# Optimization experiments

Hardware: AMD Instinct MI355X
Metric: run time of the kernel (lower is better)

The kernel has to match this reference:

```python
import jax, jax.numpy as jnp
import numpy as np

B, S, E, H, DK, DV, DF = 4, 2048, 512, 8, 64, 64, 2048
EPS = 1e-3  # keras LayerNormalization default epsilon


def setup_inputs() -> dict:
    key = jax.random.key(0)
    ks = jax.random.split(key, 24)
    def n(k, shape, scale=0.02):
        return jax.random.normal(k, shape, jnp.float32) * scale
    inp = {}
    inp["x"] = jax.random.normal(ks[0], (B, S, E), jnp.float32)
    inp["encoder_output"] = jax.random.normal(ks[1], (B, S, E), jnp.float32)
    # lookahead mask: 1 above the diagonal (masked), broadcast over batch/heads
    inp["lookahead_mask"] = jnp.triu(jnp.ones((S, S), jnp.int32), k=1)[None, None]
    # padding mask: 0 = keep (no padding in this synthetic batch)
    inp["padding_mask"] = jnp.zeros((B, 1, 1, S), jnp.int32)
    # self-attention params
    inp["sa_Wq"] = n(ks[2], (E, H * DK)); inp["sa_bq"] = jnp.zeros((H * DK,), jnp.float32)
    inp["sa_Wk"] = n(ks[3], (E, H * DK)); inp["sa_bk"] = jnp.zeros((H * DK,), jnp.float32)
    inp["sa_Wv"] = n(ks[4], (E, H * DV)); inp["sa_bv"] = jnp.zeros((H * DV,), jnp.float32)
    inp["sa_Wo"] = n(ks[5], (H * DV, E)); inp["sa_bo"] = jnp.zeros((E,), jnp.float32)
    # cross-attention params
    inp["ca_Wq"] = n(ks[6], (E, H * DK)); inp["ca_bq"] = jnp.zeros((H * DK,), jnp.float32)
    inp["ca_Wk"] = n(ks[7], (E, H * DK)); inp["ca_bk"] = jnp.zeros((H * DK,), jnp.float32)
    inp["ca_Wv"] = n(ks[8], (E, H * DV)); inp["ca_bv"] = jnp.zeros((H * DV,), jnp.float32)
    inp["ca_Wo"] = n(ks[9], (H * DV, E)); inp["ca_bo"] = jnp.zeros((E,), jnp.float32)
    # feed-forward params
    inp["ff_W1"] = n(ks[10], (E, DF)); inp["ff_b1"] = jnp.zeros((DF,), jnp.float32)
    inp["ff_W2"] = n(ks[11], (DF, E)); inp["ff_b2"] = jnp.zeros((E,), jnp.float32)
    # layernorm params (3 add&norm blocks)
    for i in (1, 2, 3):
        inp[f"ln{i}_g"] = jnp.ones((E,), jnp.float32)
        inp[f"ln{i}_b"] = jnp.zeros((E,), jnp.float32)
    return inp


def _mha(q_in, k_in, v_in, mask, Wq, bq, Wk, bk, Wv, bv, Wo, bo):
    Bq, Sq, _ = q_in.shape
    Sk = k_in.shape[1]
    q = (q_in @ Wq + bq).reshape(Bq, Sq, H, DK).transpose(0, 2, 1, 3)  # bhqd
    k = (k_in @ Wk + bk).reshape(Bq, Sk, H, DK).transpose(0, 2, 1, 3)  # bhkd
    v = (v_in @ Wv + bv).reshape(Bq, Sk, H, DV).transpose(0, 2, 1, 3)  # bhkd
    scores = jnp.einsum("bhqd,bhkd->bhqk", q, k) / jnp.sqrt(jnp.float32(DK))
    scores = scores - 1e9 * mask.astype(scores.dtype)  # additive mask (1 = masked)
    attn = jax.nn.softmax(scores, axis=-1)
    out = jnp.einsum("bhqk,bhkd->bhqd", attn, v)
    out = out.transpose(0, 2, 1, 3).reshape(Bq, Sq, H * DV)
    return out @ Wo + bo


def _add_norm(x, sub, g, b):
    y = x + sub
    m = jnp.mean(y, axis=-1, keepdims=True)
    v = jnp.var(y, axis=-1, keepdims=True)
    return (y - m) / jnp.sqrt(v + EPS) * g + b


def reference(x, encoder_output, lookahead_mask, padding_mask,
              sa_Wq, sa_bq, sa_Wk, sa_bk, sa_Wv, sa_bv, sa_Wo, sa_bo,
              ca_Wq, ca_bq, ca_Wk, ca_bk, ca_Wv, ca_bv, ca_Wo, ca_bo,
              ff_W1, ff_b1, ff_W2, ff_b2,
              ln1_g, ln1_b, ln2_g, ln2_b, ln3_g, ln3_b):
    # dropout is identity at inference (training=False)
    a1 = _mha(x, x, x, lookahead_mask,
              sa_Wq, sa_bq, sa_Wk, sa_bk, sa_Wv, sa_bv, sa_Wo, sa_bo)
    x1 = _add_norm(x, a1, ln1_g, ln1_b)
    a2 = _mha(x1, encoder_output, encoder_output, padding_mask,
              ca_Wq, ca_bq, ca_Wk, ca_bk, ca_Wv, ca_bv, ca_Wo, ca_bo)
    x2 = _add_norm(x1, a2, ln2_g, ln2_b)
    ff = jax.nn.relu(x2 @ ff_W1 + ff_b1) @ ff_W2 + ff_b2
    return _add_norm(x2, ff, ln3_g, ln3_b)
```

## Files before the change

kernel.cpp:

```cpp
#include <hip/hip_runtime.h>

#define Bx  4
#define Sx  2048
#define Ex  512
#define Hx  8
#define Tt  (Bx * Sx)

typedef short          short8 __attribute__((ext_vector_type(8)));
typedef float          f32x4  __attribute__((ext_vector_type(4)));
typedef unsigned short u16;

__device__ __forceinline__ u16 f2bf(float f) {
    unsigned int u = __float_as_uint(f);
    u += 0x7fffu + ((u >> 16) & 1u);
    return (u16)(u >> 16);
}
__device__ __forceinline__ float bf2f(u16 h) {
    return __uint_as_float(((unsigned int)h) << 16);
}

__global__ __launch_bounds__(256) void f32_to_bf16_2(const float* __restrict__ a,
                                                     const float* __restrict__ b,
                                                     u16* __restrict__ oa,
                                                     u16* __restrict__ ob)
{
    const float* in  = blockIdx.y ? b : a;
    u16*         out = blockIdx.y ? ob : oa;
    int i = (blockIdx.x * 256 + threadIdx.x) << 2;
    float4 v = *(const float4*)(in + i);
    ushort4 o;
    o.x = f2bf(v.x); o.y = f2bf(v.y); o.z = f2bf(v.z); o.w = f2bf(v.w);
    *(ushort4*)(out + i) = o;
}

__global__ __launch_bounds__(256) void transpose_bf16(const float* __restrict__ W,
                                                      u16* __restrict__ Wt,
                                                      int K, int N)
{
    __shared__ u16 tile[32][33];
    const int n0 = blockIdx.x * 32, k0 = blockIdx.y * 32;
    const int tx = threadIdx.x & 31, ty = threadIdx.x >> 5;
#pragma unroll
    for (int i = 0; i < 32; i += 8)
        tile[ty + i][tx] = f2bf(W[(size_t)(k0 + ty + i) * N + n0 + tx]);
    __syncthreads();
#pragma unroll
    for (int i = 0; i < 32; i += 8)
        Wt[(size_t)(n0 + ty + i) * K + k0 + tx] = tile[tx][ty + i];
}

struct WPtrs { const float* w[8]; };
__global__ __launch_bounds__(256) void transpose8_bf16(WPtrs ws, u16* __restrict__ base)
{
    __shared__ u16 tile[32][33];
    const float* W  = ws.w[blockIdx.z];
    u16*         Wt = base + (size_t)blockIdx.z * 262144;
    const int n0 = blockIdx.x * 32, k0 = blockIdx.y * 32;
    const int tx = threadIdx.x & 31, ty = threadIdx.x >> 5;
#pragma unroll
    for (int i = 0; i < 32; i += 8)
        tile[ty + i][tx] = f2bf(W[(size_t)(k0 + ty + i) * 512 + n0 + tx]);
    __syncthreads();
#pragma unroll
    for (int i = 0; i < 32; i += 8)
        Wt[(size_t)(n0 + ty + i) * 512 + k0 + tx] = tile[tx][ty + i];
}

template<int OUT_BF16, int RELU>
__global__ __launch_bounds__(256) void gemm128(const u16* __restrict__ A,
                                               const u16* __restrict__ Bt,
                                               const float* __restrict__ b0,
                                               const float* __restrict__ b1,
                                               const float* __restrict__ b2,
                                               const float* __restrict__ b3,
                                               void* __restrict__ Cout,
                                               int M, int N, int K, int ldc)
{
    __shared__ u16 As[128 * 40];
    __shared__ u16 Bs[128 * 40];

    const int tid  = threadIdx.x;
    const int w    = tid >> 6;
    const int lane = tid & 63;
    const int c    = lane & 15;
    const int quad = lane >> 4;
    const int wr   = w >> 1, wc = w & 1;
    const int m0   = blockIdx.y * 128;
    const int n0   = blockIdx.x * 128;

    const int row0 = tid >> 2;
    const int kc   = (tid & 3) << 3;

    const u16* Ap = A  + (size_t)(m0 + row0) * K + kc;
    const u16* Bp = Bt + (size_t)(n0 + row0) * K + kc;
    const size_t rstep = (size_t)64 * K;

    f32x4 acc[4][4];
#pragma unroll
    for (int i = 0; i < 4; i++)
#pragma unroll
        for (int j = 0; j < 4; j++) { acc[i][j][0]=0.f; acc[i][j][1]=0.f; acc[i][j][2]=0.f; acc[i][j][3]=0.f; }

    short8 ra0 = *(const short8*)(Ap);
    short8 ra1 = *(const short8*)(Ap + rstep);
    short8 rb0 = *(const short8*)(Bp);
    short8 rb1 = *(const short8*)(Bp + rstep);

    for (int k0 = 0; k0 < K; k0 += 32) {
        __syncthreads();
        *(short8*)&As[row0 * 40 + kc]        = ra0;
        *(short8*)&As[(row0 + 64) * 40 + kc] = ra1;
        *(short8*)&Bs[row0 * 40 + kc]        = rb0;
        *(short8*)&Bs[(row0 + 64) * 40 + kc] = rb1;
        __syncthreads();

        if (k0 + 32 < K) {
            ra0 = *(const short8*)(Ap + k0 + 32);
            ra1 = *(const short8*)(Ap + rstep + k0 + 32);
            rb0 = *(const short8*)(Bp + k0 + 32);
            rb1 = *(const short8*)(Bp + rstep + k0 + 32);
        }

        short8 af[4], bf[4];
#pragma unroll
        for (int i = 0; i < 4; i++)
            af[i] = *(const short8*)&As[(wr * 64 + i * 16 + c) * 40 + quad * 8];
#pragma unroll
        for (int j = 0; j < 4; j++)
            bf[j] = *(const short8*)&Bs[(wc * 64 + j * 16 + c) * 40 + quad * 8];
#pragma unroll
        for (int i = 0; i < 4; i++)
#pragma unroll
            for (int j = 0; j < 4; j++)
                acc[i][j] = __builtin_amdgcn_mfma_f32_16x16x32_bf16(af[i], bf[j], acc[i][j], 0, 0, 0);
    }

    const int seg = n0 >> 9;
    const float* bp = seg == 0 ? b0 : (seg == 1 ? b1 : (seg == 2 ? b2 : b3));
    const int nbase = n0 & 511;
    float bv[4];
#pragma unroll
    for (int j = 0; j < 4; j++) bv[j] = bp[nbase + wc * 64 + j * 16 + c];

#pragma unroll
    for (int i = 0; i < 4; i++) {
#pragma unroll
        for (int j = 0; j < 4; j++) {
            int colg = n0 + wc * 64 + j * 16 + c;
#pragma unroll
            for (int r = 0; r < 4; r++) {
                int rowg = m0 + wr * 64 + i * 16 + quad * 4 + r;
                float v = acc[i][j][r] + bv[j];
                if (RELU) v = fmaxf(v, 0.f);
                if (OUT_BF16) ((u16*)Cout)[(size_t)rowg * ldc + colg] = f2bf(v);
                else          ((float*)Cout)[(size_t)rowg * ldc + colg] = v;
            }
        }
    }
}

template<int OUT_BF16, int RELU>
__global__ __launch_bounds__(128) void gemm64(const u16* __restrict__ A,
                                              const u16* __restrict__ Bt,
                                              const float* __restrict__ bias,
                                              void* __restrict__ Cout,
                                              int M, int N, int K, int ldc)
{
    __shared__ u16 As[128 * 40];
    __shared__ u16 Bs[64 * 40];

    const int tid  = threadIdx.x;
    const int w    = tid >> 6;
    const int lane = tid & 63;
    const int c    = lane & 15;
    const int quad = lane >> 4;
    const int m0   = blockIdx.y * 128;
    const int n0   = blockIdx.x * 64;

    const int rA = tid >> 2;
    const int kc = (tid & 3) << 3;

    const u16* Ap = A  + (size_t)(m0 + rA) * K + kc;
    const u16* Bp = Bt + (size_t)(n0 + rA) * K + kc;
    const size_t a32 = (size_t)32 * K;

    f32x4 acc[4][4];
#pragma unroll
    for (int i = 0; i < 4; i++)
#pragma unroll
        for (int j = 0; j < 4; j++) { acc[i][j][0]=0.f; acc[i][j][1]=0.f; acc[i][j][2]=0.f; acc[i][j][3]=0.f; }

    short8 ra[4], rb[2];
#pragma unroll
    for (int i = 0; i < 4; i++) ra[i] = *(const short8*)(Ap + i * a32);
#pragma unroll
    for (int i = 0; i < 2; i++) rb[i] = *(const short8*)(Bp + i * a32);

    for (int k0 = 0; k0 < K; k0 += 32) {
        __syncthreads();
#pragma unroll
        for (int i = 0; i < 4; i++) *(short8*)&As[(rA + i * 32) * 40 + kc] = ra[i];
#pragma unroll
        for (int i = 0; i < 2; i++) *(short8*)&Bs[(rA + i * 32) * 40 + kc] = rb[i];
        __syncthreads();

        if (k0 + 32 < K) {
#pragma unroll
            for (int i = 0; i < 4; i++) ra[i] = *(const short8*)(Ap + i * a32 + k0 + 32);
#pragma unroll
            for (int i = 0; i < 2; i++) rb[i] = *(const short8*)(Bp + i * a32 + k0 + 32);
        }

        short8 af[4], bf[4];
#pragma unroll
        for (int i = 0; i < 4; i++)
            af[i] = *(const short8*)&As[(w * 64 + i * 16 + c) * 40 + quad * 8];
#pragma unroll
        for (int j = 0; j < 4; j++)
            bf[j] = *(const short8*)&Bs[(j * 16 + c) * 40 + quad * 8];
#pragma unroll
        for (int i = 0; i < 4; i++)
#pragma unroll
            for (int j = 0; j < 4; j++)
                acc[i][j] = __builtin_amdgcn_mfma_f32_16x16x32_bf16(af[i], bf[j], acc[i][j], 0, 0, 0);
    }

    float bv[4];
#pragma unroll
    for (int j = 0; j < 4; j++) bv[j] = bias[n0 + j * 16 + c];

#pragma unroll
    for (int i = 0; i < 4; i++) {
#pragma unroll
        for (int j = 0; j < 4; j++) {
            int colg = n0 + j * 16 + c;
#pragma unroll
            for (int r = 0; r < 4; r++) {
                int rowg = m0 + w * 64 + i * 16 + quad * 4 + r;
                float v = acc[i][j][r] + bv[j];
                if (RELU) v = fmaxf(v, 0.f);
                if (OUT_BF16) ((u16*)Cout)[(size_t)rowg * ldc + colg] = f2bf(v);
                else          ((float*)Cout)[(size_t)rowg * ldc + colg] = v;
            }
        }
    }
}

template<bool CAUSAL>
__global__ __launch_bounds__(256) void attn_mfma(const u16* __restrict__ Q,
                                                 const u16* __restrict__ K,
                                                 const u16* __restrict__ V,
                                                 u16* __restrict__ O,
                                                 int ldq, int ldk, int ldv)
{
    __shared__ u16 Klds[2][64 * 72];
    __shared__ u16 Vtlds[2][64 * 72];

    const int tid  = threadIdx.x;
    const int w    = tid >> 6;
    const int lane = tid & 63;
    const int c    = lane & 15;
    const int quad = lane >> 4;

    const int flat = blockIdx.y * 16 + blockIdx.x;
    const int idx  = flat >> 3;
    const int bh   = (flat & 7) * 4 + (idx >> 4);
    const int q0   = (idx & 15) * 128;

    const int b    = bh >> 3;
    const int h    = bh & 7;
    const int bS   = b * Sx;
    const int hoff = h * 64;
    const int qw   = q0 + w * 32;

    const int kkey = tid >> 3;
    const int kc8  = (tid & 7) << 3;
    const int vdim = tid & 63;
    const int vq   = tid >> 6;
    const int vp   = vq << 3;
    int vkey[8];
#pragma unroll
    for (int j = 0; j < 8; j++) vkey[j] = ((j & 4) << 2) + (vq << 2) + (j & 3);

    short8 qa[2][2];
#pragma unroll
    for (int a = 0; a < 2; a++) {
        const u16* qp = Q + (size_t)(bS + qw + a * 16 + c) * ldq + hoff;
        qa[a][0] = *(const short8*)(qp + quad * 8);
        qa[a][1] = *(const short8*)(qp + 32 + quad * 8);
    }

    f32x4 of[2][4];
#pragma unroll
    for (int a = 0; a < 2; a++)
#pragma unroll
        for (int f = 0; f < 4; f++) { of[a][f][0]=0.f; of[a][f][1]=0.f; of[a][f][2]=0.f; of[a][f][3]=0.f; }
    float lpart[2] = {0.f, 0.f};

    const int kend = CAUSAL ? (q0 + 128) : Sx;

    const u16* Kgp = K + (size_t)(bS + kkey) * ldk + hoff + kc8;
    const u16* Vgp = V + (size_t)bS * ldv + hoff + vdim;
    const size_t k32 = (size_t)32 * ldk;

    {
        short8 kr0 = *(const short8*)(Kgp);
        short8 kr1 = *(const short8*)(Kgp + k32);
        union { short8 v; u16 u[8]; } vb0, vb1;
#pragma unroll
        for (int j = 0; j < 8; j++) vb0.u[j] = Vgp[(size_t)vkey[j] * ldv];
#pragma unroll
        for (int j = 0; j < 8; j++) vb1.u[j] = Vgp[(size_t)(32 + vkey[j]) * ldv];
        *(short8*)&Klds[0][kkey * 72 + kc8]        = kr0;
        *(short8*)&Klds[0][(kkey + 32) * 72 + kc8] = kr1;
        *(short8*)&Vtlds[0][vdim * 72 + vp]        = vb0.v;
        *(short8*)&Vtlds[0][vdim * 72 + 32 + vp]   = vb1.v;
    }
    __syncthreads();

    int cur = 0;
    for (int kt = 0; kt < kend; kt += 64) {
        const bool more = (kt + 64 < kend);

        short8 kr0, kr1;
        union { short8 v; u16 u[8]; } vb0, vb1;
        if (more) {
            const u16* kp = Kgp + (size_t)(kt + 64) * ldk;
            kr0 = *(const short8*)(kp);
            kr1 = *(const short8*)(kp + k32);
#pragma unroll
            for (int j = 0; j < 8; j++)
                vb0.u[j] = Vgp[(size_t)(kt + 64 + vkey[j]) * ldv];
#pragma unroll
            for (int j = 0; j < 8; j++)
                vb1.u[j] = Vgp[(size_t)(kt + 96 + vkey[j]) * ldv];
        }

        int fm0 = 4, fm1 = 4;
        if (CAUSAL) {
            int d0 = ((qw + 15 - kt) >> 4) + 1;
            int d1 = ((qw + 31 - kt) >> 4) + 1;
            fm0 = d0 < 0 ? 0 : (d0 > 4 ? 4 : d0);
            fm1 = d1 < 0 ? 0 : (d1 > 4 ? 4 : d1);
        }

        if (fm1 > 0) {
            f32x4 s[2][4];
#pragma unroll
            for (int f = 0; f < 4; f++) {
                if (f < fm1) {
                    short8 kb0 = *(const short8*)&Klds[cur][(f * 16 + c) * 72 + quad * 8];
                    short8 kb1 = *(const short8*)&Klds[cur][(f * 16 + c) * 72 + 32 + quad * 8];
#pragma unroll
                    for (int a = 0; a < 2; a++) {
                        const int fma_ = a ? fm1 : fm0;
                        if (f < fma_) {
                            f32x4 z; z[0]=0.f; z[1]=0.f; z[2]=0.f; z[3]=0.f;
                            z = __builtin_amdgcn_mfma_f32_16x16x32_bf16(kb0, qa[a][0], z, 0, 0, 0);
                            z = __builtin_amdgcn_mfma_f32_16x16x32_bf16(kb1, qa[a][1], z, 0, 0, 0);
                            s[a][f] = z;
                        }
                    }
                }
            }

            union { unsigned int u[4]; short8 s8; } paA[2], paB[2];
#pragma unroll
            for (int a = 0; a < 2; a++) {
                const int fma_ = a ? fm1 : fm0;
                const int qg = qw + a * 16 + c;
#pragma unroll
                for (int f = 0; f < 4; f++) {
                    u16 pb[4];
#pragma unroll
                    for (int r = 0; r < 4; r++) {
                        float p = 0.f;
                        int kg = kt + f * 16 + quad * 4 + r;
                        if (f < fma_ && !(CAUSAL && kg > qg))
                            p = __expf(s[a][f][r] * 0.125f);
                        pb[r] = f2bf(p);
                        lpart[a] += bf2f(pb[r]);
                    }
                    unsigned int w0 = (unsigned int)pb[0] | ((unsigned int)pb[1] << 16);
                    unsigned int w1 = (unsigned int)pb[2] | ((unsigned int)pb[3] << 16);
                    if (f < 2) { paA[a].u[f * 2] = w0; paA[a].u[f * 2 + 1] = w1; }
                    else       { paB[a].u[(f - 2) * 2] = w0; paB[a].u[(f - 2) * 2 + 1] = w1; }
                }
            }

#pragma unroll
            for (int f2 = 0; f2 < 4; f2++) {
                short8 vb0f = *(const short8*)&Vtlds[cur][(f2 * 16 + c) * 72 + quad * 8];
                short8 vb1f = *(const short8*)&Vtlds[cur][(f2 * 16 + c) * 72 + 32 + quad * 8];
                if (fm0 > 0)
                    of[0][f2] = __builtin_amdgcn_mfma_f32_16x16x32_bf16(paA[0].s8, vb0f, of[0][f2], 0, 0, 0);
                of[1][f2] = __builtin_amdgcn_mfma_f32_16x16x32_bf16(paA[1].s8, vb0f, of[1][f2], 0, 0, 0);
                if (fm0 > 2)
                    of[0][f2] = __builtin_amdgcn_mfma_f32_16x16x32_bf16(paB[0].s8, vb1f, of[0][f2], 0, 0, 0);
                if (fm1 > 2)
                    of[1][f2] = __builtin_amdgcn_mfma_f32_16x16x32_bf16(paB[1].s8, vb1f, of[1][f2], 0, 0, 0);
            }
        }

        if (more) {
            *(short8*)&Klds[cur ^ 1][kkey * 72 + kc8]        = kr0;
            *(short8*)&Klds[cur ^ 1][(kkey + 32) * 72 + kc8] = kr1;
            *(short8*)&Vtlds[cur ^ 1][vdim * 72 + vp]        = vb0.v;
            *(short8*)&Vtlds[cur ^ 1][vdim * 72 + 32 + vp]   = vb1.v;
        }
        __syncthreads();
        cur ^= 1;
    }

    float rinv[2][4];
#pragma unroll
    for (int a = 0; a < 2; a++) {
        float D = lpart[a];
        D += __shfl_xor(D, 16, 64);
        D += __shfl_xor(D, 32, 64);
        float rcp = 1.f / D;
#pragma unroll
        for (int r = 0; r < 4; r++)
            rinv[a][r] = __shfl(rcp, quad * 4 + r, 64);
    }

    u16* Ob = O + (size_t)(bS + qw) * Ex + hoff;
#pragma unroll
    for (int a = 0; a < 2; a++)
#pragma unroll
        for (int f = 0; f < 4; f++)
#pragma unroll
            for (int r = 0; r < 4; r++)
                Ob[(size_t)(a * 16 + quad * 4 + r) * Ex + f * 16 + c] =
                    f2bf(of[a][f][r] * rinv[a][r]);
}

__global__ __launch_bounds__(256) void ln_add(const float* __restrict__ x,
                                              const float* __restrict__ s,
                                              const float* __restrict__ g,
                                              const float* __restrict__ bta,
                                              float* __restrict__ out,
                                              u16* __restrict__ out_bf)
{
    __shared__ float red[8];
    const int    row  = blockIdx.x;
    const int    t    = threadIdx.x;
    const size_t base = (size_t)row * Ex;

    float2 xv = *(const float2*)(x + base + (t << 1));
    float2 sv = *(const float2*)(s + base + (t << 1));
    float  y0 = xv.x + sv.x;
    float  y1 = xv.y + sv.y;

    float sum = y0 + y1;
    float sq  = y0 * y0 + y1 * y1;
#pragma unroll
    for (int o = 32; o > 0; o >>= 1) {
        sum += __shfl_down(sum, o, 64);
        sq  += __shfl_down(sq,  o, 64);
    }
    const int wid = t >> 6, lane = t & 63;
    if (lane == 0) { red[wid] = sum; red[4 + wid] = sq; }
    __syncthreads();
    if (t == 0) {
        red[0] = red[0] + red[1] + red[2] + red[3];
        red[4] = red[4] + red[5] + red[6] + red[7];
    }
    __syncthreads();

    const float mean = red[0] * (1.f / 512.f);
    const float var  = red[4] * (1.f / 512.f) - mean * mean;
    const float rstd = rsqrtf(var + 1e-3f);

    float2 gv = *(const float2*)(g   + (t << 1));
    float2 bv = *(const float2*)(bta + (t << 1));
    float  o0 = (y0 - mean) * rstd * gv.x + bv.x;
    float  o1 = (y1 - mean) * rstd * gv.y + bv.y;
    *(float2*)(out + base + (t << 1)) = make_float2(o0, o1);
    if (out_bf) {
        ushort2 ob; ob.x = f2bf(o0); ob.y = f2bf(o1);
        *(ushort2*)(out_bf + base + (t << 1)) = ob;
    }
}

extern "C" void kernel_launch(void* const* d_in, const int* in_sizes, int n_in,
                              void* d_out, int out_size, void* d_ws, size_t ws_size,
                              hipStream_t stream)
{
    const float* x     = (const float*)d_in[0];
    const float* enc   = (const float*)d_in[1];
    const float* sa_Wq = (const float*)d_in[4],  *sa_bq = (const float*)d_in[5];
    const float* sa_Wk = (const float*)d_in[6],  *sa_bk = (const float*)d_in[7];
    const float* sa_Wv = (const float*)d_in[8],  *sa_bv = (const float*)d_in[9];
    const float* sa_Wo = (const float*)d_in[10], *sa_bo = (const float*)d_in[11];
    const float* ca_Wq = (const float*)d_in[12], *ca_bq = (const float*)d_in[13];
    const float* ca_Wk = (const float*)d_in[14], *ca_bk = (const float*)d_in[15];
    const float* ca_Wv = (const float*)d_in[16], *ca_bv = (const float*)d_in[17];
    const float* ca_Wo = (const float*)d_in[18], *ca_bo = (const float*)d_in[19];
    const float* ff_W1 = (const float*)d_in[20], *ff_b1 = (const float*)d_in[21];
    const float* ff_W2 = (const float*)d_in[22], *ff_b2 = (const float*)d_in[23];
    const float* ln1_g = (const float*)d_in[24], *ln1_b = (const float*)d_in[25];
    const float* ln2_g = (const float*)d_in[26], *ln2_b = (const float*)d_in[27];
    const float* ln3_g = (const float*)d_in[28], *ln3_b = (const float*)d_in[29];

    char* ws = (char*)d_ws;
    const size_t MB = 1024 * 1024;
    u16*   bw   = (u16*)(ws);
    u16*   xb   = (u16*)(ws + 8  * MB);
    u16*   encb = (u16*)(ws + 16 * MB);
    u16*   qkvB = (u16*)(ws + 24 * MB);
    u16*   qb   = (u16*)(ws + 24 * MB);
    u16*   kvB  = (u16*)(ws + 32 * MB);
    u16*   ff1b = (u16*)(ws + 24 * MB);
    u16*   ob   = (u16*)(ws + 48 * MB);
    float* projF= (float*)(ws + 56 * MB);
    float* x1f  = (float*)(ws + 72 * MB);
    u16*   x1b  = (u16*)(ws + 88 * MB);
    u16*   x2b  = (u16*)(ws + 88 * MB);
    float* x2f  = (float*)(ws + 8  * MB);

    u16* wsaq = bw;
    u16* wsao = bw + 786432;
    u16* wcaq = bw + 1048576;
    u16* wcak = bw + 1310720;
    u16* wcao = bw + 1835008;
    u16* wff1 = bw + 2097152;
    u16* wff2 = bw + 3145728;

    f32_to_bf16_2<<<dim3(Tt * Ex / 1024, 2), dim3(256), 0, stream>>>(x, enc, xb, encb);
    WPtrs wp; wp.w[0]=sa_Wq; wp.w[1]=sa_Wk; wp.w[2]=sa_Wv; wp.w[3]=sa_Wo;
    wp.w[4]=ca_Wq; wp.w[5]=ca_Wk; wp.w[6]=ca_Wv; wp.w[7]=ca_Wo;
    transpose8_bf16<<<dim3(16, 16, 8), dim3(256), 0, stream>>>(wp, bw);
    transpose_bf16<<<dim3(64, 16), dim3(256), 0, stream>>>(ff_W1, wff1, 512, 2048);
    transpose_bf16<<<dim3(16, 64), dim3(256), 0, stream>>>(ff_W2, wff2, 2048, 512);

    auto G128 = [&](const u16* A, const u16* Wt, const float* b0, const float* b1,
                    const float* b2, const float* b3, void* C,
                    int N, int K, int ldc, int out_bf, int relu) {
        dim3 grid(N / 128, Tt / 128);
        if (out_bf) {
            if (relu) gemm128<1,1><<<grid, dim3(256), 0, stream>>>(A, Wt, b0,b1,b2,b3, C, Tt, N, K, ldc);
            else      gemm128<1,0><<<grid, dim3(256), 0, stream>>>(A, Wt, b0,b1,b2,b3, C, Tt, N, K, ldc);
        } else        gemm128<0,0><<<grid, dim3(256), 0, stream>>>(A, Wt, b0,b1,b2,b3, C, Tt, N, K, ldc);
    };
    auto G64 = [&](const u16* A, const u16* Wt, const float* bi, void* C,
                   int K, int ldc, int out_bf) {
        dim3 grid(512 / 64, Tt / 128);
        if (out_bf) gemm64<1,0><<<grid, dim3(128), 0, stream>>>(A, Wt, bi, C, Tt, 512, K, ldc);
        else        gemm64<0,0><<<grid, dim3(128), 0, stream>>>(A, Wt, bi, C, Tt, 512, K, ldc);
    };
    const dim3 agrid(Sx / 128, Bx * Hx);

    G128(xb, wsaq, sa_bq, sa_bk, sa_bv, sa_bv, qkvB, 1536, 512, 1536, 1, 0);
    attn_mfma<true><<<agrid, dim3(256), 0, stream>>>(qkvB, qkvB + 512, qkvB + 1024,
                                                     ob, 1536, 1536, 1536);
    G64(ob, wsao, sa_bo, projF, 512, 512, 0);
    ln_add<<<dim3(Tt), dim3(256), 0, stream>>>(x, projF, ln1_g, ln1_b, x1f, x1b);

    G64(x1b, wcaq, ca_bq, qb, 512, 512, 1);
    G128(encb, wcak, ca_bk, ca_bv, ca_bv, ca_bv, kvB, 1024, 512, 1024, 1, 0);
    attn_mfma<false><<<agrid, dim3(256), 0, stream>>>(qb, kvB, kvB + 512,
                                                      ob, 512, 1024, 1024);
    G64(ob, wcao, ca_bo, projF, 512, 512, 0);
    ln_add<<<dim3(Tt), dim3(256), 0, stream>>>(x1f, projF, ln2_g, ln2_b, x2f, x2b);

    G128(x2b, wff1, ff_b1, ff_b1 + 512, ff_b1 + 1024, ff_b1 + 1536,
         ff1b, 2048, 512, 2048, 1, 1);
    G64(ff1b, wff2, ff_b2, projF, 2048, 512, 0);
    ln_add<<<dim3(Tt), dim3(256), 0, stream>>>(x2f, projF, ln3_g, ln3_b,
                                               (float*)d_out, (u16*)nullptr);
}
```

Before: 495.2 us.

## Halve attention query tile to 64 rows with 128-thread blocks, packed bf16 convert

The attention kernel now processes 64 query rows per block with 2 waves (128 threads) instead of 128 rows with 4 waves. The grid doubles, and each thread loads twice as many K/V chunks into LDS per 64-key tile. This gives finer causal load balancing and more blocks per CU, at the cost of reloading K/V once per smaller query tile. The softmax probability packing also switches to the hardware v_cvt_pk_bf16_f32 instruction in place of manual rounding.

Result: no change. 500.1 us (+1.0%).

```diff
diff --git a/kernel.cpp b/kernel.cpp
--- a/kernel.cpp
+++ b/kernel.cpp
@@ -17,6 +17,11 @@
 }
 __device__ __forceinline__ float bf2f(u16 h) {
     return __uint_as_float(((unsigned int)h) << 16);
+}
+__device__ __forceinline__ unsigned int cvt_pk_bf16(float lo, float hi) {
+    unsigned int r;
+    asm("v_cvt_pk_bf16_f32 %0, %1, %2" : "=v"(r) : "v"(lo), "v"(hi));
+    return r;
 }
 
 __global__ __launch_bounds__(256) void f32_to_bf16_2(const float* __restrict__ a,
@@ -247,7 +252,7 @@
 }
 
 template<bool CAUSAL>
-__global__ __launch_bounds__(256) void attn_mfma(const u16* __restrict__ Q,
+__global__ __launch_bounds__(128) void attn_mfma(const u16* __restrict__ Q,
                                                  const u16* __restrict__ K,
                                                  const u16* __restrict__ V,
                                                  u16* __restrict__ O,
@@ -262,10 +267,10 @@
     const int c    = lane & 15;
     const int quad = lane >> 4;
 
-    const int flat = blockIdx.y * 16 + blockIdx.x;
+    const int flat = blockIdx.y * 32 + blockIdx.x;
     const int idx  = flat >> 3;
-    const int bh   = (flat & 7) * 4 + (idx >> 4);
-    const int q0   = (idx & 15) * 128;
+    const int bh   = (flat & 7) * 4 + (idx >> 5);
+    const int q0   = (idx & 31) * 64;
 
     const int b    = bh >> 3;
     const int h    = bh & 7;
@@ -276,11 +281,7 @@
     const int kkey = tid >> 3;
     const int kc8  = (tid & 7) << 3;
     const int vdim = tid & 63;
-    const int vq   = tid >> 6;
-    const int vp   = vq << 3;
-    int vkey[8];
-#pragma unroll
-    for (int j = 0; j < 8; j++) vkey[j] = ((j & 4) << 2) + (vq << 2) + (j & 3);
+    const int vg   = tid >> 6;
 
     short8 qa[2][2];
 #pragma unroll
@@ -297,24 +298,32 @@
         for (int f = 0; f < 4; f++) { of[a][f][0]=0.f; of[a][f][1]=0.f; of[a][f][2]=0.f; of[a][f][3]=0.f; }
     float lpart[2] = {0.f, 0.f};
 
-    const int kend = CAUSAL ? (q0 + 128) : Sx;
+    const int kend = CAUSAL ? (q0 + 64) : Sx;
 
     const u16* Kgp = K + (size_t)(bS + kkey) * ldk + hoff + kc8;
     const u16* Vgp = V + (size_t)bS * ldv + hoff + vdim;
-    const size_t k32 = (size_t)32 * ldk;
+    const size_t k16 = (size_t)16 * ldk;
 
     {
-        short8 kr0 = *(const short8*)(Kgp);
-        short8 kr1 = *(const short8*)(Kgp + k32);
-        union { short8 v; u16 u[8]; } vb0, vb1;
-#pragma unroll
-        for (int j = 0; j < 8; j++) vb0.u[j] = Vgp[(size_t)vkey[j] * ldv];
-#pragma unroll
-        for (int j = 0; j < 8; j++) vb1.u[j] = Vgp[(size_t)(32 + vkey[j]) * ldv];
-        *(short8*)&Klds[0][kkey * 72 + kc8]        = kr0;
-        *(short8*)&Klds[0][(kkey + 32) * 72 + kc8] = kr1;
-        *(short8*)&Vtlds[0][vdim * 72 + vp]        = vb0.v;
-        *(short8*)&Vtlds[0][vdim * 72 + 32 + vp]   = vb1.v;
+        short8 kr[4];
+#pragma unroll
+        for (int j = 0; j < 4; j++) kr[j] = *(const short8*)(Kgp + (size_t)j * k16);
+        union { short8 v; u16 u[8]; } vb[4];
+#pragma unroll
+        for (int gi = 0; gi < 4; gi++) {
+            const int gg = vg + gi * 2;
+#pragma unroll
+            for (int j = 0; j < 8; j++) {
+                int key = ((gg >> 2) << 5) + ((j & 4) << 2) + ((gg & 3) << 2) + (j & 3);
+                vb[gi].u[j] = Vgp[(size_t)key * ldv];
+            }
+        }
+#pragma unroll
+        for (int j = 0; j < 4; j++)
+            *(short8*)&Klds[0][(kkey + 16 * j) * 72 + kc8] = kr[j];
+#pragma unroll
+        for (int gi = 0; gi < 4; gi++)
+            *(short8*)&Vtlds[0][vdim * 72 + (vg + gi * 2) * 8] = vb[gi].v;
     }
     __syncthreads();
 
@@ -322,18 +331,21 @@
     for (int kt = 0; kt < kend; kt += 64) {
         const bool more = (kt + 64 < kend);
 
-        short8 kr0, kr1;
-        union { short8 v; u16 u[8]; } vb0, vb1;
+        short8 kr[4];
+        union { short8 v; u16 u[8]; } vb[4];
         if (more) {
             const u16* kp = Kgp + (size_t)(kt + 64) * ldk;
-            kr0 = *(const short8*)(kp);
-            kr1 = *(const short8*)(kp + k32);
-#pragma unroll
-            for (int j = 0; j < 8; j++)
-                vb0.u[j] = Vgp[(size_t)(kt + 64 + vkey[j]) * ldv];
-#pragma unroll
-            for (int j = 0; j < 8; j++)
-                vb1.u[j] = Vgp[(size_t)(kt + 96 + vkey[j]) * ldv];
+#pragma unroll
+            for (int j = 0; j < 4; j++) kr[j] = *(const short8*)(kp + (size_t)j * k16);
+#pragma unroll
+            for (int gi = 0; gi < 4; gi++) {
+                const int gg = vg + gi * 2;
+#pragma unroll
+                for (int j = 0; j < 8; j++) {
+                    int key = kt + 64 + ((gg >> 2) << 5) + ((j & 4) << 2) + ((gg & 3) << 2) + (j & 3);
+                    vb[gi].u[j] = Vgp[(size_t)key * ldv];
+                }
+            }
         }
 
         int fm0 = 4, fm1 = 4;
@@ -371,18 +383,19 @@
                 const int qg = qw + a * 16 + c;
 #pragma unroll
                 for (int f = 0; f < 4; f++) {
-                    u16 pb[4];
+                    float p[4];
 #pragma unroll
                     for (int r = 0; r < 4; r++) {
-                        float p = 0.f;
+                        float pv = 0.f;
                         int kg = kt + f * 16 + quad * 4 + r;
                         if (f < fma_ && !(CAUSAL && kg > qg))
-                            p = __expf(s[a][f][r] * 0.125f);
-                        pb[r] = f2bf(p);
-                        lpart[a] += bf2f(pb[r]);
+                            pv = __expf(s[a][f][r] * 0.125f);
+                        p[r] = pv;
                     }
-                    unsigned int w0 = (unsigned int)pb[0] | ((unsigned int)pb[1] << 16);
-                    unsigned int w1 = (unsigned int)pb[2] | ((unsigned int)pb[3] << 16);
+                    unsigned int w0 = cvt_pk_bf16(p[0], p[1]);
+                    unsigned int w1 = cvt_pk_bf16(p[2], p[3]);
+                    lpart[a] += __uint_as_float(w0 << 16) + __uint_as_float(w0 & 0xffff0000u);
+                    lpart[a] += __uint_as_float(w1 << 16) + __uint_as_float(w1 & 0xffff0000u);
                     if (f < 2) { paA[a].u[f * 2] = w0; paA[a].u[f * 2 + 1] = w1; }
                     else       { paB[a].u[(f - 2) * 2] = w0; paB[a].u[(f - 2) * 2 + 1] = w1; }
                 }
@@ -403,10 +416,12 @@
         }
 
         if (more) {
-            *(short8*)&Klds[cur ^ 1][kkey * 72 + kc8]        = kr0;
-            *(short8*)&Klds[cur ^ 1][(kkey + 32) * 72 + kc8] = kr1;
-            *(short8*)&Vtlds[cur ^ 1][vdim * 72 + vp]        = vb0.v;
-            *(short8*)&Vtlds[cur ^ 1][vdim * 72 + 32 + vp]   = vb1.v;
+#pragma unroll
+            for (int j = 0; j < 4; j++)
+                *(short8*)&Klds[cur ^ 1][(kkey + 16 * j) * 72 + kc8] = kr[j];
+#pragma unroll
+            for (int gi = 0; gi < 4; gi++)
+                *(short8*)&Vtlds[cur ^ 1][vdim * 72 + (vg + gi * 2) * 8] = vb[gi].v;
         }
         __syncthreads();
         cur ^= 1;
@@ -549,17 +564,17 @@
         if (out_bf) gemm64<1,0><<<grid, dim3(128), 0, stream>>>(A, Wt, bi, C, Tt, 512, K, ldc);
         else        gemm64<0,0><<<grid, dim3(128), 0, stream>>>(A, Wt, bi, C, Tt, 512, K, ldc);
     };
-    const dim3 agrid(Sx / 128, Bx * Hx);
+    const dim3 agrid(Sx / 64, Bx * Hx);
 
     G128(xb, wsaq, sa_bq, sa_bk, sa_bv, sa_bv, qkvB, 1536, 512, 1536, 1, 0);
-    attn_mfma<true><<<agrid, dim3(256), 0, stream>>>(qkvB, qkvB + 512, qkvB + 1024,
+    attn_mfma<true><<<agrid, dim3(128), 0, stream>>>(qkvB, qkvB + 512, qkvB + 1024,
                                                      ob, 1536, 1536, 1536);
     G64(ob, wsao, sa_bo, projF, 512, 512, 0);
     ln_add<<<dim3(Tt), dim3(256), 0, stream>>>(x, projF, ln1_g, ln1_b, x1f, x1b);
 
     G64(x1b, wcaq, ca_bq, qb, 512, 512, 1);
     G128(encb, wcak, ca_bk, ca_bv, ca_bv, ca_bv, kvB, 1024, 512, 1024, 1, 0);
-    attn_mfma<false><<<agrid, dim3(256), 0, stream>>>(qb, kvB, kvB + 512,
+    attn_mfma<false><<<agrid, dim3(128), 0, stream>>>(qb, kvB, kvB + 512,
                                                       ob, 512, 1024, 1024);
     G64(ob, wcao, ca_bo, projF, 512, 512, 0);
     ln_add<<<dim3(Tt), dim3(256), 0, stream>>>(x1f, projF, ln2_g, ln2_b, x2f, x2b);
```
